# Kernel tuning notes

Hardware: AMD Instinct MI355X
Metric: run time of the kernel (lower is better)

Reference implementation:

```python
import jax, jax.numpy as jnp
import numpy as np


def _kan_layer(comb, W1, b1, W2, b2, Wc, bc):
    # comb: [B, D]; W1,b1,W2: [D, K]; b2: [D]; Wc: [D, H]; bc: [H]
    # per-feature MLP: Linear(1,K) -> ReLU -> Linear(K,1), batched over D
    h = jax.nn.relu(comb[:, :, None] * W1[None, :, :] + b1[None, :, :])  # [B, D, K]
    u = jnp.einsum('bdk,dk->bd', h, W2) + b2[None, :]                    # [B, D]
    return u @ Wc + bc[None, :]                                          # [B, H]


def setup_inputs() -> dict:
    key = jax.random.key(0)
    ks = jax.random.split(key, 9)
    B, I, H, K = 2048, 256, 512, 32
    D = I + H
    s = 0.05
    return {
        'x': jax.random.normal(ks[0], (B, I), dtype=jnp.float32),
        'h_prev': jax.random.normal(ks[1], (B, H), dtype=jnp.float32),
        'c_prev': jax.random.normal(ks[2], (B, H), dtype=jnp.float32),
        'W1': jax.random.normal(ks[3], (4, D, K), dtype=jnp.float32) * s,
        'b1': jax.random.normal(ks[4], (4, D, K), dtype=jnp.float32) * s,
        'W2': jax.random.normal(ks[5], (4, D, K), dtype=jnp.float32) * s,
        'b2': jax.random.normal(ks[6], (4, D), dtype=jnp.float32) * s,
        'Wc': jax.random.normal(ks[7], (4, D, H), dtype=jnp.float32) * s,
        'bc': jax.random.normal(ks[8], (4, H), dtype=jnp.float32) * s,
    }


def reference(x, h_prev, c_prev, W1, b1, W2, b2, Wc, bc):
    comb = jnp.concatenate([x, h_prev], axis=1)  # [B, D]
    # gate order: 0=forget, 1=input, 2=output, 3=cell
    gates = [_kan_layer(comb, W1[g], b1[g], W2[g], b2[g], Wc[g], bc[g])
             for g in range(4)]
    f_t = jax.nn.sigmoid(gates[0])
    i_t = jax.nn.sigmoid(gates[1])
    o_t = jax.nn.sigmoid(gates[2])
    c_tilde = jnp.tanh(gates[3])
    c_t = f_t * c_prev + i_t * c_tilde
    h_t = o_t * jnp.tanh(c_t)
    return (h_t, c_t)
```

## Files before the change

### kernel.cpp

```cpp
#include <hip/hip_runtime.h>
#include <hip/hip_fp16.h>

#define B_  2048
#define I_  256
#define H_  512
#define D_  768
#define K_  32

typedef unsigned short ushort_t;
typedef unsigned int uint_t;
typedef __attribute__((ext_vector_type(8))) __bf16 bf16x8;
typedef __attribute__((ext_vector_type(4))) float f32x4;

__device__ __forceinline__ ushort_t f2bf(float f) {
  uint_t u = __float_as_uint(f);
  u += 0x7fffu + ((u >> 16) & 1u);
  return (ushort_t)(u >> 16);
}
__device__ __forceinline__ float fast_sigmoid(float x) {
  return 1.f / (1.f + __expf(-x));
}
__device__ __forceinline__ float fast_tanh(float x) {
  float t = __expf(2.f * fabsf(x));
  float r = 1.f - 2.f / (t + 1.f);
  return copysignf(r, x);
}
__device__ __forceinline__ void gload16(const void* g, void* l) {
  __builtin_amdgcn_global_load_lds(
      (const __attribute__((address_space(1))) void*)g,
      (__attribute__((address_space(3))) void*)l, 16, 0, 0);
}
__device__ __forceinline__ __half2 pk_max(__half2 a, __half2 b) {
  __half2 r;
  asm("v_pk_max_f16 %0, %1, %2" : "=v"(r) : "v"(a), "v"(b));
  return r;
}

__global__ __launch_bounds__(256) void transpose_all(
    const float* __restrict__ W1, const float* __restrict__ b1,
    const float* __restrict__ W2, const float* __restrict__ Wc,
    __half2* __restrict__ w1h, __half2* __restrict__ b1h, __half2* __restrict__ w2h,
    ushort_t* __restrict__ wcT) {
  __shared__ float t[32][33];
  int tx = threadIdx.x & 31, ty = threadIdx.x >> 5;
  int bid = blockIdx.x;
  if (bid < 288) {
    int z = bid / 96;
    int g = (bid / 24) % 4;
    int d0 = (bid % 24) * 32;
    const float* src = (z == 0) ? W1 : (z == 1) ? b1 : W2;
    __half2* dst     = (z == 0) ? w1h : (z == 1) ? b1h : w2h;
#pragma unroll
    for (int i = 0; i < 4; ++i) {
      int r = ty + i * 8;
      t[r][tx] = src[((size_t)g * D_ + d0 + r) * K_ + tx];
    }
    __syncthreads();
#pragma unroll
    for (int i = 0; i < 2; ++i) {
      int r2 = ty + i * 8;
      __half2 v = __halves2half2(__float2half_rn(t[tx][2 * r2]),
                                 __float2half_rn(t[tx][2 * r2 + 1]));
      dst[((size_t)g * (K_ / 2) + r2) * D_ + d0 + tx] = v;
    }
  } else {
    int r2 = bid - 288;
    int g = r2 / 384;
    int rem = r2 % 384;
    int d0 = (rem / 16) * 32;
    int h0 = (rem % 16) * 32;
#pragma unroll
    for (int i = 0; i < 4; ++i) {
      int r = ty + i * 8;
      t[r][tx] = Wc[((size_t)g * D_ + d0 + r) * H_ + h0 + tx];
    }
    __syncthreads();
#pragma unroll
    for (int i = 0; i < 4; ++i) {
      int r = ty + i * 8;
      wcT[((size_t)g * H_ + h0 + r) * D_ + d0 + tx] = f2bf(t[tx][r]);
    }
  }
}

__global__ __launch_bounds__(256) void kan_mlp(
    const float* __restrict__ x, const float* __restrict__ hp,
    const __half2* __restrict__ w1h, const __half2* __restrict__ b1h,
    const __half2* __restrict__ w2h, const float* __restrict__ b2,
    ushort_t* __restrict__ uT) {
  int bi = blockIdx.x;
  int combo = bi >> 7;
  int bc = bi & 127;
  int g = combo & 3;
  int dc = combo >> 2;
  int t = threadIdx.x;
  int d = dc * 256 + t;

  const float* src = (dc == 0) ? (x + t) : (hp + ((dc == 1) ? t : t + 256));
  int stride = (dc == 0) ? I_ : H_;
  int b0 = bc * 16;

  __half2 w1c[16], b1c[16], w2c[16];
  const __half2* w1p = w1h + (size_t)g * (K_ / 2) * D_ + d;
  const __half2* b1p = b1h + (size_t)g * (K_ / 2) * D_ + d;
  const __half2* w2p = w2h + (size_t)g * (K_ / 2) * D_ + d;
#pragma unroll
  for (int kp = 0; kp < 16; ++kp) {
    w1c[kp] = w1p[(size_t)kp * D_];
    b1c[kp] = b1p[(size_t)kp * D_];
    w2c[kp] = w2p[(size_t)kp * D_];
  }
  float bias = b2[(size_t)g * D_ + d];
  const __half2 z2 = __halves2half2(__float2half_rn(0.f), __float2half_rn(0.f));
  ushort_t* up = uT + (size_t)g * B_ * D_ + (size_t)b0 * D_ + d;

#pragma unroll 1
  for (int jc = 0; jc < 2; ++jc) {
    __half2 cv2[8], acc2[8];
#pragma unroll
    for (int j = 0; j < 8; ++j) {
      float c = src[(size_t)(b0 + jc * 8 + j) * stride];
      cv2[j] = __half2half2(__float2half_rn(c));
      acc2[j] = z2;
    }
#pragma unroll
    for (int kp = 0; kp < 16; ++kp)
#pragma unroll
      for (int j = 0; j < 8; ++j) {
        __half2 t2 = __hfma2(cv2[j], w1c[kp], b1c[kp]);
        acc2[j] = __hfma2(pk_max(t2, z2), w2c[kp], acc2[j]);
      }
#pragma unroll
    for (int j = 0; j < 8; ++j) {
      float u = bias + __half2float(__low2half(acc2[j])) +
                __half2float(__high2half(acc2[j]));
      up[(size_t)(jc * 8 + j) * D_] = f2bf(u);
    }
  }
}

#define TBM 64
#define THN 64
#define BK2 32
#define NT2 (D_ / BK2)
#define AREG 16384
#define BUF2 32768
#define NBUF2 4

__global__ __launch_bounds__(1024, 4) void kan_phase2(
    const ushort_t* __restrict__ uT, const ushort_t* __restrict__ wcT,
    const float* __restrict__ bc, const float* __restrict__ cprev,
    float* __restrict__ out) {
  __shared__ __align__(16) char smem[NBUF2 * BUF2];
  const int b0 = blockIdx.x * TBM;
  const int h0 = blockIdx.y * THN;
  const int t = threadIdx.x;
  const int w = t >> 6;
  const int l = t & 63;
  const int g = w >> 2, mh = w & 3;
  const int frow = l & 15, c0 = l >> 4;

  const int srow = t >> 2, sc = t & 3;
  const int sg = srow >> 6, sr = srow & 63;
  const int scg = sc ^ ((sr ^ (sr >> 2)) & 3);
  const ushort_t* asrc = uT + ((size_t)sg * B_ + b0 + sr) * D_ + scg * 8;
  const ushort_t* bsrc = wcT + ((size_t)sg * H_ + h0 + sr) * D_ + scg * 8;
  const int aLds = t * 16;
  const int bLds = AREG + t * 16;

  const int key = (frow ^ (frow >> 2)) & 3;
  const int cx = ((c0 ^ key) << 4);
  const int aoff = ((g * 64 + mh * 16 + frow) << 6) + cx;
  int boff[4];
#pragma unroll
  for (int n = 0; n < 4; ++n)
    boff[n] = AREG + ((g * 64 + n * 16 + frow) << 6) + cx;

  f32x4 acc[4];
#pragma unroll
  for (int n = 0; n < 4; ++n) {
    float bv = bc[(size_t)g * H_ + h0 + n * 16 + frow];
    acc[n] = (f32x4){bv, bv, bv, bv};
  }

  auto stage = [&](int bufoff, int ke) {
    gload16(asrc + ke, smem + bufoff + aLds);
    gload16(bsrc + ke, smem + bufoff + bLds);
  };
  auto compute = [&](const char* bb) {
    bf16x8 af = *(const bf16x8*)(bb + aoff);
    bf16x8 bf[4];
#pragma unroll
    for (int n = 0; n < 4; ++n) bf[n] = *(const bf16x8*)(bb + boff[n]);
    __builtin_amdgcn_s_setprio(1);
#pragma unroll
    for (int n = 0; n < 4; ++n)
      acc[n] = __builtin_amdgcn_mfma_f32_16x16x32_bf16(af, bf[n], acc[n], 0, 0, 0);
    __builtin_amdgcn_s_setprio(0);
  };

  stage(0 * BUF2, 0 * BK2);
  stage(1 * BUF2, 1 * BK2);
  stage(2 * BUF2, 2 * BK2);
  int s = 0;
  for (; s < NT2 - 3; ++s) {
    asm volatile("s_waitcnt vmcnt(4)" ::: "memory");
    __builtin_amdgcn_s_barrier();
    stage(((s + 3) & 3) * BUF2, (s + 3) * BK2);
    compute(smem + (s & 3) * BUF2);
  }
  asm volatile("s_waitcnt vmcnt(4)" ::: "memory");
  __builtin_amdgcn_s_barrier();
  compute(smem + (s & 3) * BUF2);
  ++s;
  asm volatile("s_waitcnt vmcnt(2)" ::: "memory");
  __builtin_amdgcn_s_barrier();
  compute(smem + (s & 3) * BUF2);
  ++s;
  asm volatile("s_waitcnt vmcnt(0)" ::: "memory");
  __builtin_amdgcn_s_barrier();
  compute(smem + (s & 3) * BUF2);
  __syncthreads();

  float* gf = (float*)smem;
#pragma unroll
  for (int n = 0; n < 4; ++n)
#pragma unroll
    for (int e = 0; e < 4; ++e) {
      int row = mh * 16 + c0 * 4 + e;
      int col = n * 16 + frow;
      gf[((size_t)g * 64 + row) * 68 + col] = acc[n][e];
    }
  __syncthreads();

  {
    int row = t >> 4;
    int ch = t & 15;
    int b = b0 + row;
    int hc = h0 + ch * 4;
    f32x4 g0 = *(const f32x4*)&gf[((size_t)0 * 64 + row) * 68 + ch * 4];
    f32x4 g1 = *(const f32x4*)&gf[((size_t)1 * 64 + row) * 68 + ch * 4];
    f32x4 g2 = *(const f32x4*)&gf[((size_t)2 * 64 + row) * 68 + ch * 4];
    f32x4 g3 = *(const f32x4*)&gf[((size_t)3 * 64 + row) * 68 + ch * 4];
    f32x4 cp = *(const f32x4*)&cprev[(size_t)b * H_ + hc];
    f32x4 hv, cv;
#pragma unroll
    for (int e = 0; e < 4; ++e) {
      float ft = fast_sigmoid(g0[e]);
      float it = fast_sigmoid(g1[e]);
      float ot = fast_sigmoid(g2[e]);
      float tc = fast_tanh(g3[e]);
      float cn = ft * cp[e] + it * tc;
      cv[e] = cn;
      hv[e] = ot * fast_tanh(cn);
    }
    *(f32x4*)&out[(size_t)b * H_ + hc] = hv;
    *(f32x4*)&out[(size_t)B_ * H_ + (size_t)b * H_ + hc] = cv;
  }
}

extern "C" void kernel_launch(void* const* d_in, const int* in_sizes, int n_in,
                              void* d_out, int out_size, void* d_ws, size_t ws_size,
                              hipStream_t stream) {
  const float* x  = (const float*)d_in[0];
  const float* hp = (const float*)d_in[1];
  const float* cp = (const float*)d_in[2];
  const float* W1 = (const float*)d_in[3];
  const float* b1 = (const float*)d_in[4];
  const float* W2 = (const float*)d_in[5];
  const float* b2 = (const float*)d_in[6];
  const float* Wc = (const float*)d_in[7];
  const float* bc = (const float*)d_in[8];
  float* out = (float*)d_out;

  __half2* w1h = (__half2*)d_ws;
  __half2* b1h = w1h + (size_t)4 * (K_ / 2) * D_;
  __half2* w2h = b1h + (size_t)4 * (K_ / 2) * D_;
  ushort_t* wcT = (ushort_t*)(w2h + (size_t)4 * (K_ / 2) * D_);
  ushort_t* uT  = wcT + (size_t)4 * H_ * D_;

  transpose_all<<<1824, 256, 0, stream>>>(W1, b1, W2, Wc, w1h, b1h, w2h, wcT);
  kan_mlp<<<1536, 256, 0, stream>>>(x, hp, w1h, b1h, w2h, b2, uT);
  kan_phase2<<<dim3(B_ / TBM, H_ / THN), 1024, 0, stream>>>(uT, wcT, bc, cp, out);
}
```

Baseline: 46.44 us.

## Halve phase2 block to 512 threads with 2x4 MFMA tiles per wave and double buffering

```diff
diff --git a/kernel.cpp b/kernel.cpp
--- a/kernel.cpp
+++ b/kernel.cpp
@@ -145,117 +145,131 @@
 #define NT2 (D_ / BK2)
 #define AREG 16384
 #define BUF2 32768
-#define NBUF2 4
-
-__global__ __launch_bounds__(1024, 4) void kan_phase2(
+
+__global__ __launch_bounds__(512, 4) void kan_phase2(
     const ushort_t* __restrict__ uT, const ushort_t* __restrict__ wcT,
     const float* __restrict__ bc, const float* __restrict__ cprev,
     float* __restrict__ out) {
-  __shared__ __align__(16) char smem[NBUF2 * BUF2];
+  __shared__ __align__(16) char smem[2 * BUF2];
   const int b0 = blockIdx.x * TBM;
   const int h0 = blockIdx.y * THN;
   const int t = threadIdx.x;
   const int w = t >> 6;
   const int l = t & 63;
-  const int g = w >> 2, mh = w & 3;
+  const int g = w >> 1, mh2 = w & 1;
   const int frow = l & 15, c0 = l >> 4;
 
-  const int srow = t >> 2, sc = t & 3;
-  const int sg = srow >> 6, sr = srow & 63;
-  const int scg = sc ^ ((sr ^ (sr >> 2)) & 3);
-  const ushort_t* asrc = uT + ((size_t)sg * B_ + b0 + sr) * D_ + scg * 8;
-  const ushort_t* bsrc = wcT + ((size_t)sg * H_ + h0 + sr) * D_ + scg * 8;
-  const int aLds = t * 16;
-  const int bLds = AREG + t * 16;
+  const ushort_t* asrc[2];
+  const ushort_t* bsrc[2];
+  int aLds[2], bLds[2];
+#pragma unroll
+  for (int i = 0; i < 2; ++i) {
+    int s = t + i * 512;
+    int srow = s >> 2, sc = s & 3;
+    int sg = srow >> 6, sr = srow & 63;
+    int scg = sc ^ ((sr ^ (sr >> 2)) & 3);
+    asrc[i] = uT + ((size_t)sg * B_ + b0 + sr) * D_ + scg * 8;
+    bsrc[i] = wcT + ((size_t)sg * H_ + h0 + sr) * D_ + scg * 8;
+    aLds[i] = s * 16;
+    bLds[i] = AREG + s * 16;
+  }
 
   const int key = (frow ^ (frow >> 2)) & 3;
   const int cx = ((c0 ^ key) << 4);
-  const int aoff = ((g * 64 + mh * 16 + frow) << 6) + cx;
-  int boff[4];
+  int aoff[2], boff[4];
+#pragma unroll
+  for (int m = 0; m < 2; ++m)
+    aoff[m] = ((g * 64 + mh2 * 32 + m * 16 + frow) << 6) + cx;
 #pragma unroll
   for (int n = 0; n < 4; ++n)
     boff[n] = AREG + ((g * 64 + n * 16 + frow) << 6) + cx;
 
-  f32x4 acc[4];
+  f32x4 acc[2][4];
 #pragma unroll
   for (int n = 0; n < 4; ++n) {
     float bv = bc[(size_t)g * H_ + h0 + n * 16 + frow];
-    acc[n] = (f32x4){bv, bv, bv, bv};
+#pragma unroll
+    for (int m = 0; m < 2; ++m) acc[m][n] = (f32x4){bv, bv, bv, bv};
   }
 
   auto stage = [&](int bufoff, int ke) {
-    gload16(asrc + ke, smem + bufoff + aLds);
-    gload16(bsrc + ke, smem + bufoff + bLds);
+#pragma unroll
+    for (int i = 0; i < 2; ++i) gload16(asrc[i] + ke, smem + bufoff + aLds[i]);
+#pragma unroll
+    for (int i = 0; i < 2; ++i) gload16(bsrc[i] + ke, smem + bufoff + bLds[i]);
   };
   auto compute = [&](const char* bb) {
-    bf16x8 af = *(const bf16x8*)(bb + aoff);
-    bf16x8 bf[4];
+    bf16x8 af[2], bf[4];
+#pragma unroll
+    for (int m = 0; m < 2; ++m) af[m] = *(const bf16x8*)(bb + aoff[m]);
 #pragma unroll
     for (int n = 0; n < 4; ++n) bf[n] = *(const bf16x8*)(bb + boff[n]);
     __builtin_amdgcn_s_setprio(1);
 #pragma unroll
-    for (int n = 0; n < 4; ++n)
-      acc[n] = __builtin_amdgcn_mfma_f32_16x16x32_bf16(af, bf[n], acc[n], 0, 0, 0);
+    for (int m = 0; m < 2; ++m)
+#pragma unroll
+      for (int n = 0; n < 4; ++n)
+        acc[m][n] = __builtin_amdgcn_mfma_f32_16x16x32_bf16(af[m], bf[n], acc[m][n], 0, 0, 0);
     __builtin_amdgcn_s_setprio(0);
   };
 
-  stage(0 * BUF2, 0 * BK2);
-  stage(1 * BUF2, 1 * BK2);
-  stage(2 * BUF2, 2 * BK2);
-  int s = 0;
-  for (; s < NT2 - 3; ++s) {
-    asm volatile("s_waitcnt vmcnt(4)" ::: "memory");
+  stage(0, 0 * BK2);
+  stage(BUF2, 1 * BK2);
+  for (int s = 0; s < NT2; ++s) {
+    if (s + 1 < NT2)
+      asm volatile("s_waitcnt vmcnt(4)" ::: "memory");
+    else
+      asm volatile("s_waitcnt vmcnt(0)" ::: "memory");
     __builtin_amdgcn_s_barrier();
-    stage(((s + 3) & 3) * BUF2, (s + 3) * BK2);
-    compute(smem + (s & 3) * BUF2);
-  }
-  asm volatile("s_waitcnt vmcnt(4)" ::: "memory");
-  __builtin_amdgcn_s_barrier();
-  compute(smem + (s & 3) * BUF2);
-  ++s;
-  asm volatile("s_waitcnt vmcnt(2)" ::: "memory");
-  __builtin_amdgcn_s_barrier();
-  compute(smem + (s & 3) * BUF2);
-  ++s;
-  asm volatile("s_waitcnt vmcnt(0)" ::: "memory");
-  __builtin_amdgcn_s_barrier();
-  compute(smem + (s & 3) * BUF2);
+    compute(smem + (s & 1) * BUF2);
+    if (s + 2 < NT2) {
+      __builtin_amdgcn_s_barrier();
+      stage((s & 1) * BUF2, (s + 2) * BK2);
+    }
+  }
   __syncthreads();
 
   float* gf = (float*)smem;
-#pragma unroll
-  for (int n = 0; n < 4; ++n)
-#pragma unroll
-    for (int e = 0; e < 4; ++e) {
-      int row = mh * 16 + c0 * 4 + e;
-      int col = n * 16 + frow;
-      gf[((size_t)g * 64 + row) * 68 + col] = acc[n][e];
-    }
-  __syncthreads();
-
-  {
-    int row = t >> 4;
-    int ch = t & 15;
-    int b = b0 + row;
-    int hc = h0 + ch * 4;
-    f32x4 g0 = *(const f32x4*)&gf[((size_t)0 * 64 + row) * 68 + ch * 4];
-    f32x4 g1 = *(const f32x4*)&gf[((size_t)1 * 64 + row) * 68 + ch * 4];
-    f32x4 g2 = *(const f32x4*)&gf[((size_t)2 * 64 + row) * 68 + ch * 4];
-    f32x4 g3 = *(const f32x4*)&gf[((size_t)3 * 64 + row) * 68 + ch * 4];
-    f32x4 cp = *(const f32x4*)&cprev[(size_t)b * H_ + hc];
-    f32x4 hv, cv;
-#pragma unroll
-    for (int e = 0; e < 4; ++e) {
-      float ft = fast_sigmoid(g0[e]);
-      float it = fast_sigmoid(g1[e]);
-      float ot = fast_sigmoid(g2[e]);
-      float tc = fast_tanh(g3[e]);
-      float cn = ft * cp[e] + it * tc;
-      cv[e] = cn;
-      hv[e] = ot * fast_tanh(cn);
-    }
-    *(f32x4*)&out[(size_t)b * H_ + hc] = hv;
-    *(f32x4*)&out[(size_t)B_ * H_ + (size_t)b * H_ + hc] = cv;
+#pragma unroll 1
+  for (int h = 0; h < 2; ++h) {
+    if (mh2 == h) {
+#pragma unroll
+      for (int m = 0; m < 2; ++m)
+#pragma unroll
+        for (int n = 0; n < 4; ++n)
+#pragma unroll
+          for (int e = 0; e < 4; ++e) {
+            int row = m * 16 + c0 * 4 + e;
+            int col = n * 16 + frow;
+            gf[((size_t)g * 32 + row) * 68 + col] = acc[m][n][e];
+          }
+    }
+    __syncthreads();
+    {
+      int row = t >> 4;
+      int ch = t & 15;
+      int b = b0 + h * 32 + row;
+      int hc = h0 + ch * 4;
+      f32x4 g0 = *(const f32x4*)&gf[((size_t)0 * 32 + row) * 68 + ch * 4];
+      f32x4 g1 = *(const f32x4*)&gf[((size_t)1 * 32 + row) * 68 + ch * 4];
+      f32x4 g2 = *(const f32x4*)&gf[((size_t)2 * 32 + row) * 68 + ch * 4];
+      f32x4 g3 = *(const f32x4*)&gf[((size_t)3 * 32 + row) * 68 + ch * 4];
+      f32x4 cp = *(const f32x4*)&cprev[(size_t)b * H_ + hc];
+      f32x4 hv, cv;
+#pragma unroll
+      for (int e = 0; e < 4; ++e) {
+        float ft = fast_sigmoid(g0[e]);
+        float it = fast_sigmoid(g1[e]);
+        float ot = fast_sigmoid(g2[e]);
+        float tc = fast_tanh(g3[e]);
+        float cn = ft * cp[e] + it * tc;
+        cv[e] = cn;
+        hv[e] = ot * fast_tanh(cn);
+      }
+      *(f32x4*)&out[(size_t)b * H_ + hc] = hv;
+      *(f32x4*)&out[(size_t)B_ * H_ + (size_t)b * H_ + hc] = cv;
+    }
+    __syncthreads();
   }
 }
 
@@ -281,5 +295,5 @@
 
   transpose_all<<<1824, 256, 0, stream>>>(W1, b1, W2, Wc, w1h, b1h, w2h, wcT);
   kan_mlp<<<1536, 256, 0, stream>>>(x, hp, w1h, b1h, w2h, b2, uT);
-  kan_phase2<<<dim3(B_ / TBM, H_ / THN), 1024, 0, stream>>>(uT, wcT, bc, cp, out);
-}
+  kan_phase2<<<dim3(B_ / TBM, H_ / THN), 512, 0, stream>>>(uT, wcT, bc, cp, out);
+}
```

New measurement: 47.17 us. About the same (+1.6%).
